# Optimization experiments

Hardware: AMD Instinct MI355X
Metric: run time of the kernel (lower is better)

The kernel has to match this reference:

```python
import jax, jax.numpy as jnp
import numpy as np

L, B, E, H = 512, 32, 1024, 16
NEG = -1e9  # finite stand-in for masked_fill(-inf); avoids NaNs if a row were fully masked


def setup_inputs() -> dict:
    key = jax.random.key(0)
    ks = jax.random.split(key, 6)
    s_in = (2.0 / (3 * E + E)) ** 0.5   # xavier-ish scale for in_proj
    s_out = (2.0 / (E + E)) ** 0.5
    return {
        "query": jax.random.normal(ks[0], (L, B, E), jnp.float32),
        "key": jax.random.normal(ks[1], (L, B, E), jnp.float32),
        "value": jax.random.normal(ks[2], (L, B, E), jnp.float32),
        "attn_mask": jax.random.randint(ks[3], (B, L, L), 0, 2).astype(jnp.bool_),
        "in_proj_weight": jax.random.normal(ks[4], (3 * E, E), jnp.float32) * s_in,
        "in_proj_bias": jnp.zeros((3 * E,), jnp.float32),
        "out_proj_weight": jax.random.normal(ks[5], (E, E), jnp.float32) * s_out,
        "out_proj_bias": jnp.zeros((E,), jnp.float32),
        "num_heads": H,
    }


def reference(query, key, value, attn_mask, in_proj_weight, in_proj_bias,
              out_proj_weight, out_proj_bias, num_heads):
    Lq, Bz, Em = query.shape
    hd = Em // num_heads
    Wq, Wk, Wv = jnp.split(in_proj_weight, 3, axis=0)
    bq, bk, bv = jnp.split(in_proj_bias, 3, axis=0)
    # in-projection: x @ W^T + b  (torch F.linear convention)
    q = query @ Wq.T + bq
    k = key @ Wk.T + bk
    v = value @ Wv.T + bv
    # [L, B, E] -> [B*H, L, hd], batch-major (b*H + h) per torch view semantics
    def split_heads(x):
        return x.reshape(x.shape[0], Bz * num_heads, hd).transpose(1, 0, 2)
    q, k, v = split_heads(q), split_heads(k), split_heads(v)
    q = q / jnp.sqrt(jnp.asarray(hd, q.dtype))
    # scores: [B*H, Lq, Lk]
    attn = jnp.einsum('bqd,bkd->bqk', q, k)
    # mask broadcast to heads: [B, L, L] -> [B*H, L, L] with index b*H + h
    mask_mh = jnp.repeat(attn_mask, num_heads, axis=0)
    # original: scatter zeros where masked, then masked_fill(-inf) inside
    # multi_head_positional_attention; net effect = mask -> -inf before softmax
    attn = jnp.where(mask_mh, NEG, attn)
    p = jax.nn.softmax(attn, axis=-1)
    out = jnp.einsum('bqk,bkd->bqd', p, v)        # [B*H, Lq, hd]
    out = out.transpose(1, 0, 2).reshape(Lq, Bz, Em)
    out = out @ out_proj_weight.T + out_proj_bias  # [L, B, E]
    return out
```

## Files before the change

kernel.cpp:

```cpp
#include <hip/hip_runtime.h>
#include <hip/hip_bf16.h>
#include <stdint.h>

#define LSEQ 512
#define BATCH 32
#define EMB 1024
#define NHEAD 16
#define HDIM 64
#define TOK (LSEQ*BATCH)
#define BHTOT (BATCH*NHEAD)

typedef __attribute__((ext_vector_type(8))) short short8;
typedef __attribute__((ext_vector_type(4))) short short4v;
typedef __attribute__((ext_vector_type(4))) float f32x4;

__device__ __forceinline__ short f2bf(float f) {
  __hip_bfloat16 h = __float2bfloat16(f);
  union { __hip_bfloat16 h; short s; } u; u.h = h;
  return u.s;
}

__device__ __forceinline__ short8 cvt8(f32x4 x0, f32x4 x1) {
  short8 o;
  o[0] = f2bf(x0[0]); o[1] = f2bf(x0[1]); o[2] = f2bf(x0[2]); o[3] = f2bf(x0[3]);
  o[4] = f2bf(x1[0]); o[5] = f2bf(x1[1]); o[6] = f2bf(x1[2]); o[7] = f2bf(x1[3]);
  return o;
}

#if defined(__has_builtin)
#if __has_builtin(__builtin_amdgcn_global_load_lds)
#define HAVE_GLL 1
#endif
#endif

__device__ __forceinline__ void gload_lds16(const void* g, void* l) {
#ifdef HAVE_GLL
  __builtin_amdgcn_global_load_lds((const __attribute__((address_space(1))) void*)g,
                                   (__attribute__((address_space(3))) void*)l, 16, 0, 0);
#else
  *(short8*)l = *(const short8*)g;
#endif
}

#define WAIT_VM8  do { asm volatile("s_waitcnt vmcnt(8)" ::: "memory"); __builtin_amdgcn_sched_barrier(0); } while (0)
#define WAIT_VM4  do { asm volatile("s_waitcnt vmcnt(4)" ::: "memory"); __builtin_amdgcn_sched_barrier(0); } while (0)
#define WAIT_VM0  do { asm volatile("s_waitcnt vmcnt(0)" ::: "memory"); __builtin_amdgcn_sched_barrier(0); } while (0)
#define WAIT_LGKM0 do { asm volatile("s_waitcnt lgkmcnt(0)" ::: "memory"); __builtin_amdgcn_sched_barrier(0); } while (0)
#define BAR() __builtin_amdgcn_s_barrier()

__global__ __launch_bounds__(256) void castx_kernel(const float* __restrict__ xq,
                                                    const float* __restrict__ xk,
                                                    const float* __restrict__ xv,
                                                    short* __restrict__ xb)
{
  const size_t i = blockIdx.x * 256 + threadIdx.x;
  #pragma unroll
  for (int it = 0; it < 6; ++it) {
    const float* src = (it < 2) ? xq : (it < 4) ? xk : xv;
    size_t p = i + (size_t)it * 1048576;
    size_t local = p - (size_t)(it >> 1) * 2097152;
    f32x4 x0 = ((const f32x4*)src)[2 * local];
    f32x4 x1 = ((const f32x4*)src)[2 * local + 1];
    ((short8*)xb)[p] = cvt8(x0, x1);
  }
}

__global__ __launch_bounds__(256) void prep2_kernel(const float* __restrict__ W,
                                                    const float* __restrict__ Wo,
                                                    const float* __restrict__ bias,
                                                    short* __restrict__ Wb, short* __restrict__ Wob,
                                                    float* __restrict__ biasp,
                                                    const int* __restrict__ mask,
                                                    uint32_t* __restrict__ mb)
{
  const int i = blockIdx.x * 256 + threadIdx.x;
  if (i < 786432) {
    f32x4 v = ((const f32x4*)W)[i];
    int row = i >> 8;
    float s = (row < 1024) ? 0.125f : 1.0f;
    short4v o;
    o[0] = f2bf(v[0]*s); o[1] = f2bf(v[1]*s); o[2] = f2bf(v[2]*s); o[3] = f2bf(v[3]*s);
    ((short4v*)Wb)[i] = o;
  } else {
    int j = i - 786432;
    f32x4 v = ((const f32x4*)Wo)[j];
    short4v o;
    o[0] = f2bf(v[0]); o[1] = f2bf(v[1]); o[2] = f2bf(v[2]); o[3] = f2bf(v[3]);
    ((short4v*)Wob)[j] = o;
  }
  if (i < 768) {
    f32x4 v = ((const f32x4*)bias)[i];
    float s = (i < 256) ? 0.125f : 1.0f;
    f32x4 o = {v[0]*s, v[1]*s, v[2]*s, v[3]*s};
    ((f32x4*)biasp)[i] = o;
  }
  {
    int w = i >> 6;
    int lane = threadIdx.x & 63;
    const int* src = mask + ((size_t)w << 9);
    uint32_t* dst = mb + w * 16;
    #pragma unroll
    for (int c = 0; c < 8; ++c) {
      int v = src[c * 64 + lane];
      unsigned long long m = __ballot(v != 0);
      if (lane == 0) dst[c*2]     = (uint32_t)m;
      if (lane == 1) dst[c*2 + 1] = (uint32_t)(m >> 32);
    }
  }
}


#define FRAG_READ(AsX, BsX)                                           \
    short8 af[4], bfr[4];                                             \
    _Pragma("unroll")                                                 \
    for (int mi = 0; mi < 4; ++mi) {                                  \
      int row = wm + mi * 16 + l15;                                   \
      int cs = l4 ^ ((row >> 1) & 3);                                 \
      af[mi] = *(const short8*)&AsX[row * 32 + cs * 8];               \
    }                                                                 \
    _Pragma("unroll")                                                 \
    for (int ni = 0; ni < 4; ++ni) {                                  \
      int row = wn + ni * 16 + l15;                                   \
      int cs = l4 ^ ((row >> 1) & 3);                                 \
      bfr[ni] = *(const short8*)&BsX[row * 32 + cs * 8];              \
    }

#define DO_MFMA()                                                     \
    _Pragma("unroll")                                                 \
    for (int mi = 0; mi < 4; ++mi)                                    \
      _Pragma("unroll")                                               \
      for (int ni = 0; ni < 4; ++ni)                                  \
        acc[mi][ni] = __builtin_amdgcn_mfma_f32_16x16x32_bf16(af[mi], bfr[ni], acc[mi][ni], 0, 0, 0)

#define ISSUE(AsX, BsX, koff)                                         \
    _Pragma("unroll")                                                 \
    for (int jj = 0; jj < 2; ++jj) {                                  \
      gload_lds16(aSrc[jj] + (koff), &AsX[sDst[jj]]);                 \
      gload_lds16(bSrc[jj] + (koff), &BsX[sDst[jj]]);                 \
    }

#define GSTEP_I(AsX, BsX, WAITM, koff)                                \
  { WAITM; BAR();                                                     \
    FRAG_READ(AsX, BsX);                                              \
    WAIT_LGKM0; BAR();                                                \
    ISSUE(AsX, BsX, koff);                                            \
    DO_MFMA(); }

#define GSTEP_N(AsX, BsX, WAITM)                                      \
  { WAITM; BAR();                                                     \
    FRAG_READ(AsX, BsX);                                              \
    WAIT_LGKM0; BAR();                                                \
    DO_MFMA(); }

#define STAGE_COORDS(Abase, Bbase)                                    \
  const short* aSrc[2]; const short* bSrc[2]; int sDst[2];            \
  _Pragma("unroll")                                                   \
  for (int jj = 0; jj < 2; ++jj) {                                    \
    int ch = tid + jj * 256;                                          \
    int row = ch >> 2, cl = ch & 3;                                   \
    int cs = cl ^ ((row >> 1) & 3);                                   \
    aSrc[jj] = (Abase) + (size_t)(m0 + row) * 1024 + cs * 8;          \
    bSrc[jj] = (Bbase) + (size_t)(n0 + row) * 1024 + cs * 8;          \
    sDst[jj] = ch * 8;                                                \
  }

#define PIPE_BODY()                                                   \
  ISSUE(As0, Bs0, 0); ISSUE(As1, Bs1, 32); ISSUE(As2, Bs2, 64);       \
  for (int i = 0; i < 9; ++i) {                                       \
    const int s = 3 * i;                                              \
    GSTEP_I(As0, Bs0, WAIT_VM8, (s + 3) * 32);                        \
    GSTEP_I(As1, Bs1, WAIT_VM8, (s + 4) * 32);                        \
    GSTEP_I(As2, Bs2, WAIT_VM8, (s + 5) * 32);                        \
  }                                                                   \
  GSTEP_I(As0, Bs0, WAIT_VM8, 30 * 32);                               \
  GSTEP_I(As1, Bs1, WAIT_VM8, 31 * 32);                               \
  GSTEP_N(As2, Bs2, WAIT_VM8);                                        \
  GSTEP_N(As0, Bs0, WAIT_VM4);                                        \
  GSTEP_N(As1, Bs1, WAIT_VM0);

__launch_bounds__(256, 3)
__global__ void proj_gemm(const short* __restrict__ A, const short* __restrict__ B,
                          const float* __restrict__ bp, short* __restrict__ C)
{
  int flat = blockIdx.y * 8 + blockIdx.x;
  int X = flat & 7, s0 = flat >> 3;
  int m0 = (X * 16 + (s0 >> 3)) * 128;
  int n0 = (s0 & 7) * 128;

  __shared__ alignas(16) short As0[128 * 32];
  __shared__ alignas(16) short As1[128 * 32];
  __shared__ alignas(16) short As2[128 * 32];
  __shared__ alignas(16) short Bs0[128 * 32];
  __shared__ alignas(16) short Bs1[128 * 32];
  __shared__ alignas(16) short Bs2[128 * 32];

  const int tid = threadIdx.x, lane = tid & 63;
  const int w = tid >> 6;
  const int wm = (w >> 1) * 64, wn = (w & 1) * 64;
  const int l15 = lane & 15, l4 = lane >> 4;

  STAGE_COORDS(A, B);

  f32x4 acc[4][4];
  #pragma unroll
  for (int mi = 0; mi < 4; ++mi)
    #pragma unroll
    for (int ni = 0; ni < 4; ++ni) acc[mi][ni] = f32x4{0.f, 0.f, 0.f, 0.f};

  PIPE_BODY();

  #pragma unroll
  for (int ni = 0; ni < 4; ++ni) {
    int gcol = n0 + wn + ni * 16 + l15;
    float bv = bp[gcol];
    int h = gcol >> 6, d = gcol & 63;
    #pragma unroll
    for (int mi = 0; mi < 4; ++mi) {
      int growb = m0 + wm + mi * 16 + l4 * 4;
      #pragma unroll
      for (int r = 0; r < 4; ++r) {
        int grow = growb + r;
        int lsq = grow >> 5, bb = grow & 31;
        C[((size_t)((bb * NHEAD + h) * LSEQ + lsq)) * HDIM + d] = f2bf(acc[mi][ni][r] + bv);
      }
    }
  }
}

__launch_bounds__(256, 3)
__global__ void out_gemm(const short* __restrict__ Ab, const short* __restrict__ W,
                         const float* __restrict__ bo, float* __restrict__ out)
{
  int flat = blockIdx.y * 8 + blockIdx.x;
  int X = flat & 7, s0 = flat >> 3;
  int m0 = (X * 16 + (s0 >> 3)) * 128;
  int n0 = (s0 & 7) * 128;

  __shared__ alignas(16) short As0[128 * 32];
  __shared__ alignas(16) short As1[128 * 32];
  __shared__ alignas(16) short As2[128 * 32];
  __shared__ alignas(16) short Bs0[128 * 32];
  __shared__ alignas(16) short Bs1[128 * 32];
  __shared__ alignas(16) short Bs2[128 * 32];

  const int tid = threadIdx.x, lane = tid & 63;
  const int w = tid >> 6;
  const int wm = (w >> 1) * 64, wn = (w & 1) * 64;
  const int l15 = lane & 15, l4 = lane >> 4;

  STAGE_COORDS(Ab, W);

  f32x4 acc[4][4];
  #pragma unroll
  for (int mi = 0; mi < 4; ++mi)
    #pragma unroll
    for (int ni = 0; ni < 4; ++ni) acc[mi][ni] = f32x4{0.f, 0.f, 0.f, 0.f};

  PIPE_BODY();

  #pragma unroll
  for (int ni = 0; ni < 4; ++ni) {
    int gcol = n0 + wn + ni * 16 + l15;
    float bv = bo[gcol];
    #pragma unroll
    for (int mi = 0; mi < 4; ++mi) {
      int growb = m0 + wm + mi * 16 + l4 * 4;
      #pragma unroll
      for (int r = 0; r < 4; ++r)
        out[(size_t)(growb + r) * 1024 + gcol] = acc[mi][ni][r] + bv;
    }
  }
}

__launch_bounds__(256, 2)
__global__ void attn_kernel(const short* __restrict__ qh, const short* __restrict__ kh,
                            const short* __restrict__ vh, const uint32_t* __restrict__ mb,
                            short* __restrict__ ao)
{
  int flat = blockIdx.y * 8 + blockIdx.x;
  int X = flat & 7, s = flat >> 3;
  int bh = X * 64 + (s >> 2);
  int qblk = s & 3;
  int b = bh >> 4, h = bh & 15;
  int q0 = qblk * 128;

  const int tid = threadIdx.x, lane = tid & 63, w = tid >> 6;
  const int l15 = lane & 15, l4 = lane >> 4;

  __shared__ alignas(16) short Ks[64 * 64];
  __shared__ alignas(16) short Vt[64 * 72];
  __shared__ alignas(16) short Ps[4 * 32 * 72];
  __shared__ uint32_t Mw[128 * 2];

  const size_t bhoff = (size_t)bh * (LSEQ * HDIM);

  short8 aq[2][2];
  #pragma unroll
  for (int m = 0; m < 2; ++m) {
    int qrow = q0 + w * 32 + m * 16 + l15;
    const short* qp = qh + bhoff + (size_t)qrow * HDIM + l4 * 8;
    aq[m][0] = *(const short8*)qp;
    aq[m][1] = *(const short8*)(qp + 32);
  }

  f32x4 oacc[2][4];
  float l_part[2][4];
  #pragma unroll
  for (int m = 0; m < 2; ++m) {
    #pragma unroll
    for (int n = 0; n < 4; ++n) oacc[m][n] = f32x4{0.f, 0.f, 0.f, 0.f};
    #pragma unroll
    for (int r = 0; r < 4; ++r) l_part[m][r] = 0.f;
  }

  for (int kt = 0; kt < 8; ++kt) {
    __syncthreads();
    #pragma unroll
    for (int jj = 0; jj < 2; ++jj) {
      int ch = tid + jj * 256;
      int row = ch >> 3, cl = ch & 7;
      int cg = cl ^ (row & 7);
      const short* g = kh + bhoff + (size_t)(kt * 64 + row) * HDIM + cg * 8;
      gload_lds16(g, &Ks[ch * 8]);
    }
    #pragma unroll
    for (int jj = 0; jj < 2; ++jj) {
      int c = tid + jj * 256;
      int kv = c & 63, d0 = (c >> 6) * 8;
      const short* g = vh + bhoff + (size_t)(kt * 64 + kv) * HDIM + d0;
      short8 vv = *(const short8*)g;
      #pragma unroll
      for (int j = 0; j < 8; ++j) Vt[(d0 + j) * 72 + kv] = vv[j];
    }
    {
      int qr = tid >> 1, wd = tid & 1;
      Mw[qr * 2 + wd] = mb[((size_t)b * LSEQ + q0 + qr) * 16 + kt * 2 + wd];
    }
    __syncthreads();

    f32x4 sa[2][4];
    #pragma unroll
    for (int m = 0; m < 2; ++m)
      #pragma unroll
      for (int n = 0; n < 4; ++n) sa[m][n] = f32x4{0.f, 0.f, 0.f, 0.f};
    #pragma unroll
    for (int ss = 0; ss < 2; ++ss) {
      #pragma unroll
      for (int n = 0; n < 4; ++n) {
        int row = n * 16 + l15;
        int cs = (ss * 4 + l4) ^ (row & 7);
        short8 bk = *(const short8*)&Ks[row * 64 + cs * 8];
        #pragma unroll
        for (int m = 0; m < 2; ++m)
          sa[m][n] = __builtin_amdgcn_mfma_f32_16x16x32_bf16(aq[m][ss], bk, sa[m][n], 0, 0, 0);
      }
    }

    #pragma unroll
    for (int m = 0; m < 2; ++m) {
      #pragma unroll
      for (int r = 0; r < 4; ++r) {
        int qr = w * 32 + m * 16 + l4 * 4 + r;
        uint32_t w0 = Mw[qr * 2] >> l15;
        uint32_t w1 = Mw[qr * 2 + 1] >> l15;
        float p0 = (w0 & 1u)        ? 0.f : __expf(sa[m][0][r]);
        float p1 = ((w0 >> 16) & 1u) ? 0.f : __expf(sa[m][1][r]);
        float p2 = (w1 & 1u)        ? 0.f : __expf(sa[m][2][r]);
        float p3 = ((w1 >> 16) & 1u) ? 0.f : __expf(sa[m][3][r]);
        l_part[m][r] += (p0 + p1) + (p2 + p3);
        short* pp = &Ps[w * 2304 + (m * 16 + l4 * 4 + r) * 72];
        pp[0 * 16 + l15] = f2bf(p0);
        pp[1 * 16 + l15] = f2bf(p1);
        pp[2 * 16 + l15] = f2bf(p2);
        pp[3 * 16 + l15] = f2bf(p3);
      }
    }

    #pragma unroll
    for (int ss = 0; ss < 2; ++ss) {
      short8 pa[2];
      #pragma unroll
      for (int m = 0; m < 2; ++m)
        pa[m] = *(const short8*)&Ps[w * 2304 + (m * 16 + l15) * 72 + ss * 32 + l4 * 8];
      #pragma unroll
      for (int n = 0; n < 4; ++n) {
        short8 bv = *(const short8*)&Vt[(n * 16 + l15) * 72 + ss * 32 + l4 * 8];
        #pragma unroll
        for (int m = 0; m < 2; ++m)
          oacc[m][n] = __builtin_amdgcn_mfma_f32_16x16x32_bf16(pa[m], bv, oacc[m][n], 0, 0, 0);
      }
    }
  }

  #pragma unroll
  for (int m = 0; m < 2; ++m) {
    #pragma unroll
    for (int r = 0; r < 4; ++r) {
      float l = l_part[m][r];
      #pragma unroll
      for (int off = 1; off < 16; off <<= 1) l += __shfl_xor(l, off, 64);
      float inv = 1.0f / fmaxf(l, 1e-30f);
      int qrow = q0 + w * 32 + m * 16 + l4 * 4 + r;
      size_t tbase = ((size_t)qrow * BATCH + b) * EMB + h * HDIM;
      #pragma unroll
      for (int n = 0; n < 4; ++n)
        ao[tbase + n * 16 + l15] = f2bf(oacc[m][n][r] * inv);
    }
  }
}

extern "C" void kernel_launch(void* const* d_in, const int* in_sizes, int n_in,
                              void* d_out, int out_size, void* d_ws, size_t ws_size,
                              hipStream_t stream) {
  const float* q_in = (const float*)d_in[0];
  const float* k_in = (const float*)d_in[1];
  const float* v_in = (const float*)d_in[2];
  const int*   mask = (const int*)d_in[3];
  const float* Wp   = (const float*)d_in[4];
  const float* bp   = (const float*)d_in[5];
  const float* Wo   = (const float*)d_in[6];
  const float* bo   = (const float*)d_in[7];

  char* ws = (char*)d_ws;
  short* Wb    = (short*)ws;    ws += (size_t)3072 * 1024 * 2;
  short* Wob   = (short*)ws;    ws += (size_t)1024 * 1024 * 2;
  float* biasp = (float*)ws;    ws += (size_t)3072 * 4;
  uint32_t* mb = (uint32_t*)ws; ws += (size_t)BATCH * LSEQ * 16 * 4;
  short* qh    = (short*)ws;    ws += (size_t)TOK * EMB * 2;
  short* kh    = (short*)ws;    ws += (size_t)TOK * EMB * 2;
  short* vh    = (short*)ws;    ws += (size_t)TOK * EMB * 2;
  short* xb    = (short*)ws;    ws += (size_t)3 * TOK * EMB * 2;
  short* ao    = xb;

  castx_kernel<<<4096, 256, 0, stream>>>(q_in, k_in, v_in, xb);
  prep2_kernel<<<4096, 256, 0, stream>>>(Wp, Wo, bp, Wb, Wob, biasp, mask, mb);
  proj_gemm<<<dim3(8, 128), 256, 0, stream>>>(xb,                       Wb,                biasp,        qh);
  proj_gemm<<<dim3(8, 128), 256, 0, stream>>>(xb + (size_t)TOK * EMB,   Wb + 1024 * 1024,  biasp + 1024, kh);
  proj_gemm<<<dim3(8, 128), 256, 0, stream>>>(xb + (size_t)2*TOK * EMB, Wb + 2*1024*1024,  biasp + 2048, vh);
  attn_kernel<<<dim3(8, 256), 256, 0, stream>>>(qh, kh, vh, mb, ao);
  out_gemm<<<dim3(8, 128), 256, 0, stream>>>(ao, Wob, bo, (float*)d_out);
}
```

Measured before the change: 326.3 us.

## Merge QKV projection launches, use nontemporal casts, repack mask bits, raise attention occupancy

The three separate projection GEMM launches are merged into one launch with a z-dimension that selects the Q, K or V operands. The input cast kernel now uses nontemporal loads and stores to avoid polluting cache with streaming data. The mask bitpacking is permuted so each attention lane reads one word and takes a 4-bit nibble instead of two words and shifts. The attention kernel's launch bound rises from 2 to 4 blocks per SM, which may force register spills.

```diff
diff --git a/kernel.cpp b/kernel.cpp
--- a/kernel.cpp
+++ b/kernel.cpp
@@ -59,9 +59,9 @@
     const float* src = (it < 2) ? xq : (it < 4) ? xk : xv;
     size_t p = i + (size_t)it * 1048576;
     size_t local = p - (size_t)(it >> 1) * 2097152;
-    f32x4 x0 = ((const f32x4*)src)[2 * local];
-    f32x4 x1 = ((const f32x4*)src)[2 * local + 1];
-    ((short8*)xb)[p] = cvt8(x0, x1);
+    f32x4 x0 = __builtin_nontemporal_load((const f32x4*)src + 2 * local);
+    f32x4 x1 = __builtin_nontemporal_load((const f32x4*)src + 2 * local + 1);
+    __builtin_nontemporal_store(cvt8(x0, x1), (short8*)xb + p);
   }
 }
 
@@ -97,11 +97,12 @@
   {
     int w = i >> 6;
     int lane = threadIdx.x & 63;
+    int src_idx = ((lane & 3) << 4) | (lane >> 2);
     const int* src = mask + ((size_t)w << 9);
     uint32_t* dst = mb + w * 16;
     #pragma unroll
     for (int c = 0; c < 8; ++c) {
-      int v = src[c * 64 + lane];
+      int v = src[c * 64 + src_idx];
       unsigned long long m = __ballot(v != 0);
       if (lane == 0) dst[c*2]     = (uint32_t)m;
       if (lane == 1) dst[c*2 + 1] = (uint32_t)(m >> 32);
@@ -179,9 +180,17 @@
   GSTEP_N(As1, Bs1, WAIT_VM0);
 
 __launch_bounds__(256, 3)
-__global__ void proj_gemm(const short* __restrict__ A, const short* __restrict__ B,
-                          const float* __restrict__ bp, short* __restrict__ C)
+__global__ void proj_gemm(const short* __restrict__ xb, const short* __restrict__ W,
+                          const float* __restrict__ biasp,
+                          short* __restrict__ qh, short* __restrict__ kh,
+                          short* __restrict__ vh)
 {
+  int z = blockIdx.z;
+  const short* A = xb + (size_t)z * TOK * EMB;
+  short* C       = (z == 0) ? qh : (z == 1) ? kh : vh;
+  const short* B = W + (size_t)z * 1024 * 1024;
+  const float* bp = biasp + z * 1024;
+
   int flat = blockIdx.y * 8 + blockIdx.x;
   int X = flat & 7, s0 = flat >> 3;
   int m0 = (X * 16 + (s0 >> 3)) * 128;
@@ -256,7 +265,18 @@
     #pragma unroll
     for (int ni = 0; ni < 4; ++ni) acc[mi][ni] = f32x4{0.f, 0.f, 0.f, 0.f};
 
-  PIPE_BODY();
+  ISSUE(As0, Bs0, 0); ISSUE(As1, Bs1, 32); ISSUE(As2, Bs2, 64);
+  for (int i = 0; i < 9; ++i) {
+    const int s = 3 * i;
+    GSTEP_I(As0, Bs0, WAIT_VM8, (s + 3) * 32);
+    GSTEP_I(As1, Bs1, WAIT_VM8, (s + 4) * 32);
+    GSTEP_I(As2, Bs2, WAIT_VM8, (s + 5) * 32);
+  }
+  GSTEP_I(As0, Bs0, WAIT_VM8, 30 * 32);
+  GSTEP_I(As1, Bs1, WAIT_VM8, 31 * 32);
+  GSTEP_N(As2, Bs2, WAIT_VM8);
+  GSTEP_N(As0, Bs0, WAIT_VM4);
+  GSTEP_N(As1, Bs1, WAIT_VM0);
 
   #pragma unroll
   for (int ni = 0; ni < 4; ++ni) {
@@ -272,7 +292,7 @@
   }
 }
 
-__launch_bounds__(256, 2)
+__launch_bounds__(256, 4)
 __global__ void attn_kernel(const short* __restrict__ qh, const short* __restrict__ kh,
                             const short* __restrict__ vh, const uint32_t* __restrict__ mb,
                             short* __restrict__ ao)
@@ -361,12 +381,12 @@
       #pragma unroll
       for (int r = 0; r < 4; ++r) {
         int qr = w * 32 + m * 16 + l4 * 4 + r;
-        uint32_t w0 = Mw[qr * 2] >> l15;
-        uint32_t w1 = Mw[qr * 2 + 1] >> l15;
-        float p0 = (w0 & 1u)        ? 0.f : __expf(sa[m][0][r]);
-        float p1 = ((w0 >> 16) & 1u) ? 0.f : __expf(sa[m][1][r]);
-        float p2 = (w1 & 1u)        ? 0.f : __expf(sa[m][2][r]);
-        float p3 = ((w1 >> 16) & 1u) ? 0.f : __expf(sa[m][3][r]);
+        uint32_t wsel = Mw[qr * 2 + (l15 >> 3)];
+        uint32_t nib = wsel >> ((l15 & 7) * 4);
+        float p0 = (nib & 1u) ? 0.f : __expf(sa[m][0][r]);
+        float p1 = (nib & 2u) ? 0.f : __expf(sa[m][1][r]);
+        float p2 = (nib & 4u) ? 0.f : __expf(sa[m][2][r]);
+        float p3 = (nib & 8u) ? 0.f : __expf(sa[m][3][r]);
         l_part[m][r] += (p0 + p1) + (p2 + p3);
         short* pp = &Ps[w * 2304 + (m * 16 + l4 * 4 + r) * 72];
         pp[0 * 16 + l15] = f2bf(p0);
@@ -434,9 +454,7 @@
 
   castx_kernel<<<4096, 256, 0, stream>>>(q_in, k_in, v_in, xb);
   prep2_kernel<<<4096, 256, 0, stream>>>(Wp, Wo, bp, Wb, Wob, biasp, mask, mb);
-  proj_gemm<<<dim3(8, 128), 256, 0, stream>>>(xb,                       Wb,                biasp,        qh);
-  proj_gemm<<<dim3(8, 128), 256, 0, stream>>>(xb + (size_t)TOK * EMB,   Wb + 1024 * 1024,  biasp + 1024, kh);
-  proj_gemm<<<dim3(8, 128), 256, 0, stream>>>(xb + (size_t)2*TOK * EMB, Wb + 2*1024*1024,  biasp + 2048, vh);
+  proj_gemm<<<dim3(8, 128, 3), 256, 0, stream>>>(xb, Wb, biasp, qh, kh, vh);
   attn_kernel<<<dim3(8, 256), 256, 0, stream>>>(qh, kh, vh, mb, ao);
   out_gemm<<<dim3(8, 128), 256, 0, stream>>>(ao, Wob, bo, (float*)d_out);
 }
```

Result: faster. 317.5 us (-2.7%).
